# Performance work log

Hardware: AMD Instinct MI355X
Metric: run time of the kernel (lower is better)

Reference implementation:

```python
import jax, jax.numpy as jnp
import numpy as np

B, NQ, N, D_IN, D_KEY, D_MODEL = 8, 2048, 2048, 512, 512, 512


def setup_inputs() -> dict:
    key = jax.random.key(0)
    k1, k2, k3, k4, k5, k6 = jax.random.split(key, 6)
    lim_k = np.sqrt(6.0 / (D_IN + D_KEY))
    lim_v = np.sqrt(6.0 / (D_IN + D_MODEL))
    return {
        "node_features": jax.random.normal(k1, (B, N, D_IN), dtype=jnp.float32),
        "query": jax.random.normal(k2, (B, NQ, D_IN), dtype=jnp.float32),
        "mask": jax.random.bernoulli(k3, 0.3, (NQ, B, N)),  # True = masked out
        "wq": jax.random.uniform(k4, (D_IN, D_KEY), jnp.float32, -lim_k, lim_k),
        "wk": jax.random.uniform(k5, (D_IN, D_KEY), jnp.float32, -lim_k, lim_k),
        "wv": jax.random.uniform(k6, (D_IN, D_MODEL), jnp.float32, -lim_v, lim_v),
    }


def reference(node_features, query, mask, wq, wk, wv):
    # Projections
    Q = query @ wq              # [B, NQ, d_key]
    K = node_features @ wk      # [B, N, d_key]
    V = node_features @ wv      # [B, N, d_model]
    # Raw scores [B, NQ, N]
    scores = jnp.einsum("bqd,bnd->bqn", Q, K)
    b, nq, n = scores.shape
    # Faithful to tf: reshape to (NQ, B, N), mask with float32.min, reshape back
    s = scores.reshape(nq, b, n)
    masked = jnp.where(mask, jnp.finfo(jnp.float32).min, s).reshape(b, nq, n)
    # Scale AFTER masking (as in the original), then softmax over keys
    attn = jax.nn.softmax(masked / jnp.sqrt(jnp.float32(K.shape[-1])), axis=-1)
    return attn @ V             # [B, NQ, d_model]
```

## Files before the change

### kernel.cpp

```cpp
#include <hip/hip_runtime.h>

typedef __attribute__((ext_vector_type(8))) short bf16x8;
typedef __attribute__((ext_vector_type(4))) float f32x4;

__device__ __forceinline__ unsigned short f2bf(float f) {
  unsigned int u = __builtin_bit_cast(unsigned int, f);
  u += 0x7fffu + ((u >> 16) & 1u);
  return (unsigned short)(u >> 16);
}

#define GLD16(gp, lp) __builtin_amdgcn_global_load_lds( \
    (const __attribute__((address_space(1))) unsigned int*)(gp), \
    (__attribute__((address_space(3))) unsigned int*)(lp), 16, 0, 0)

__global__ __launch_bounds__(256) void pack_mask(
    const unsigned char* __restrict__ m, unsigned long long* __restrict__ pm)
{
  __shared__ int mode1;
  if (threadIdx.x == 0) mode1 = 0;
  __syncthreads();

  const int g = blockIdx.x * 256 + threadIdx.x;
  const size_t base = (size_t)g * 64;

  uint4 v[4];
  const uint4* p1 = (const uint4*)(m + base);
  v[0] = p1[0]; v[1] = p1[1]; v[2] = p1[2]; v[3] = p1[3];
  unsigned int probe = 0;
#pragma unroll
  for (int j = 0; j < 4; ++j)
    probe |= (v[j].x | v[j].y | v[j].z | v[j].w);
  if (probe & 0x0000ff00u) mode1 = 1;
  __syncthreads();

  unsigned long long bits = 0;
  if (mode1) {
#pragma unroll
    for (int j = 0; j < 4; ++j) {
      unsigned int w[4] = {v[j].x, v[j].y, v[j].z, v[j].w};
#pragma unroll
      for (int q = 0; q < 4; ++q) {
        unsigned int u = w[q];
#pragma unroll
        for (int b = 0; b < 4; ++b)
          if ((u >> (8 * b)) & 0xffu) bits |= 1ull << (j * 16 + q * 4 + b);
      }
    }
  } else {
    const uint4* p4 = (const uint4*)(m + base * 4);
#pragma unroll
    for (int j = 0; j < 16; ++j) {
      uint4 w = p4[j];
      if (w.x) bits |= 1ull << (j * 4 + 0);
      if (w.y) bits |= 1ull << (j * 4 + 1);
      if (w.z) bits |= 1ull << (j * 4 + 2);
      if (w.w) bits |= 1ull << (j * 4 + 3);
    }
  }
  pm[g] = bits;
}

__global__ void prep(const float* __restrict__ query, const float* __restrict__ node,
                     const float* __restrict__ wq, const float* __restrict__ wk,
                     const float* __restrict__ wv,
                     unsigned short* __restrict__ Xq, unsigned short* __restrict__ Xn,
                     unsigned short* __restrict__ wqb, unsigned short* __restrict__ wkb,
                     unsigned short* __restrict__ wvt, float* __restrict__ sums)
{
  const int b = blockIdx.x;
  if (b < 16384) {
    int i = b * 256 + threadIdx.x;
    const float* src;
    unsigned short* dst;
    int j;
    if (i < 2097152) { src = query; dst = Xq; j = i; }
    else             { src = node;  dst = Xn; j = i - 2097152; }
    float4 v = ((const float4*)src)[j];
    ushort4 o;
    o.x = f2bf(v.x); o.y = f2bf(v.y); o.z = f2bf(v.z); o.w = f2bf(v.w);
    ((ushort4*)dst)[j] = o;
  } else if (b < 19456) {
    int idx = (b - 16384) * 256 + threadIdx.x;
    int w = idx >> 18;
    int rem = idx & 262143;
    if (w == 0)      wqb[rem] = f2bf(wq[rem]);
    else if (w == 1) wkb[rem] = f2bf(wk[rem]);
    else {
      int n = rem >> 9, k = rem & 511;
      wvt[n * 512 + k] = f2bf(wv[k * 512 + n]);
    }
  } else {
    int idx = (b - 19456) * 256 + threadIdx.x;
    sums[idx] = 0.0f;
  }
}

__device__ __forceinline__ void core128(
    const unsigned short* __restrict__ Ab, const unsigned short* __restrict__ Bb,
    void* __restrict__ Cb, long ldA, long ldB, long ldO, int nk,
    long bm, long bn, char* smem, int mode,
    const unsigned long long* __restrict__ pmask, float* __restrict__ sumz,
    const float* __restrict__ sums_ro)
{
  const int tid = threadIdx.x;
  const int lane = tid & 63;
  const int wid = tid >> 6;
  const int wr = wid >> 1, wc = wid & 1;
  const int fr = lane & 15, fq = lane >> 4;

  const int srow = tid >> 2;
  const int sch = (tid & 3) ^ ((srow >> 1) & 3);

  char* bufs[3] = { smem, smem + 16384, smem + 32768 };

#define STAGE_C(buf, kt) do { \
    const long k0_ = (long)(kt) << 5; \
    GLD16(Ab + (bm + srow) * ldA + k0_ + sch * 8,        (buf) + tid * 16); \
    GLD16(Ab + (bm + 64 + srow) * ldA + k0_ + sch * 8,   (buf) + 4096 + tid * 16); \
    GLD16(Bb + (bn + srow) * ldB + k0_ + sch * 8,        (buf) + 8192 + tid * 16); \
    GLD16(Bb + (bn + 64 + srow) * ldB + k0_ + sch * 8,   (buf) + 12288 + tid * 16); \
  } while (0)

  int aoff[4], boff[4];
#pragma unroll
  for (int i = 0; i < 4; ++i) {
    const int ra = wr * 64 + i * 16 + fr;
    aoff[i] = ra * 64 + (fq ^ ((ra >> 1) & 3)) * 16;
    const int rb = wc * 64 + i * 16 + fr;
    boff[i] = 8192 + rb * 64 + (fq ^ ((rb >> 1) & 3)) * 16;
  }

  f32x4 acc[4][4] = {};

  STAGE_C(bufs[0], 0);
  STAGE_C(bufs[1], 1);
  char* c0 = bufs[0]; char* c1 = bufs[1]; char* c2 = bufs[2];

  for (int t = 0; t < nk; ++t) {
    __builtin_amdgcn_sched_barrier(0);
    __builtin_amdgcn_s_barrier();
    if (t + 2 < nk) {
      STAGE_C(c2, t + 2);
      asm volatile("s_waitcnt vmcnt(8)" ::: "memory");
    } else if (t + 2 == nk) {
      asm volatile("s_waitcnt vmcnt(4)" ::: "memory");
    } else {
      asm volatile("s_waitcnt vmcnt(0)" ::: "memory");
    }
    __builtin_amdgcn_s_barrier();
    __builtin_amdgcn_sched_barrier(0);

    bf16x8 a[4];
#pragma unroll
    for (int mi = 0; mi < 4; ++mi)
      a[mi] = *(const bf16x8*)(c0 + aoff[mi]);
    __builtin_amdgcn_s_setprio(1);
#pragma unroll
    for (int nj = 0; nj < 4; ++nj) {
      const bf16x8 b = *(const bf16x8*)(c0 + boff[nj]);
#pragma unroll
      for (int mi = 0; mi < 4; ++mi)
        acc[mi][nj] = __builtin_amdgcn_mfma_f32_16x16x32_bf16(a[mi], b, acc[mi][nj], 0, 0, 0);
    }
    __builtin_amdgcn_s_setprio(0);

    char* tmp = c0; c0 = c1; c1 = c2; c2 = tmp;
  }
#undef STAGE_C

  const float SCALE = 0.04419417382415922f;
  if (mode == 0) {
    unsigned short* C = (unsigned short*)Cb;
#pragma unroll
    for (int mi = 0; mi < 4; ++mi)
#pragma unroll
      for (int nj = 0; nj < 4; ++nj) {
        const long row = bm + wr * 64 + mi * 16 + fq * 4;
        const long col = bn + wc * 64 + nj * 16 + fr;
#pragma unroll
        for (int r = 0; r < 4; ++r)
          C[(row + r) * ldO + col] = f2bf(acc[mi][nj][r]);
      }
  } else if (mode == 1) {
    unsigned short* C = (unsigned short*)Cb;
    const long wword = (bn >> 6) + wc;
#pragma unroll
    for (int mi = 0; mi < 4; ++mi) {
      const long rowb = bm + wr * 64 + mi * 16 + fq * 4;
#pragma unroll
      for (int r = 0; r < 4; ++r) {
        const long row = rowb + r;
        const unsigned long long w = pmask[row * 32 + wword];
        unsigned short* Crow = C + row * ldO + bn + wc * 64 + fr;
        float s = 0.f;
#pragma unroll
        for (int nj = 0; nj < 4; ++nj) {
          const int sh = nj * 16 + fr;
          float e = ((w >> sh) & 1ull) ? 0.0f : __expf(acc[mi][nj][r] * SCALE);
          s += e;
          Crow[nj * 16] = f2bf(e);
        }
        s += __shfl_xor(s, 1); s += __shfl_xor(s, 2);
        s += __shfl_xor(s, 4); s += __shfl_xor(s, 8);
        if (fr == 0) atomicAdd(&sumz[row], s);
      }
    }
  } else {
    float* C = (float*)Cb;
#pragma unroll
    for (int mi = 0; mi < 4; ++mi) {
      const long rowb = bm + wr * 64 + mi * 16 + fq * 4;
#pragma unroll
      for (int r = 0; r < 4; ++r) {
        const long row = rowb + r;
        const float iv = 1.0f / sums_ro[row];
        const long colb = bn + wc * 64 + fr;
#pragma unroll
        for (int nj = 0; nj < 4; ++nj)
          C[row * ldO + colb + nj * 16] = acc[mi][nj][r] * iv;
      }
    }
  }
}

__global__ __launch_bounds__(256, 3) void gemm_mt(
    const unsigned short* __restrict__ wkb, const unsigned short* __restrict__ wqb,
    unsigned short* __restrict__ MT)
{
  extern __shared__ char smem[];
  core128(wkb, wqb, MT, 512, 512, 512, 16,
          (long)blockIdx.x * 128, (long)blockIdx.y * 128, smem, 0,
          nullptr, nullptr, nullptr);
}

__global__ __launch_bounds__(256, 3) void gemm_proj(
    const unsigned short* __restrict__ Xq, const unsigned short* __restrict__ Xn,
    const unsigned short* __restrict__ MT, const unsigned short* __restrict__ Wvt,
    unsigned short* __restrict__ T, unsigned short* __restrict__ Vt)
{
  extern __shared__ char smem[];
  if (blockIdx.z == 0) {
    core128(Xq, MT, T, 512, 512, 512, 16,
            (long)blockIdx.x * 128, (long)blockIdx.y * 128, smem, 0,
            nullptr, nullptr, nullptr);
  } else {
    core128(Wvt, Xn, Vt, 512, 512, 16384, 16,
            (long)blockIdx.y * 128, (long)blockIdx.x * 128, smem, 0,
            nullptr, nullptr, nullptr);
  }
}

__global__ __launch_bounds__(256, 3) void gemm_scores(
    const unsigned short* __restrict__ T, const unsigned short* __restrict__ Xn,
    unsigned short* __restrict__ Eg, const unsigned long long* __restrict__ pm,
    float* __restrict__ sums)
{
  extern __shared__ char smem[];
  const long z = blockIdx.x;
  core128(T + z * 1048576, Xn + z * 1048576, Eg + z * 4194304,
          512, 512, 2048, 16,
          (long)blockIdx.y * 128, (long)blockIdx.z * 128, smem, 1,
          pm + z * 65536, sums + z * 2048, nullptr);
}

__global__ __launch_bounds__(256, 3) void gemm_pv(
    const unsigned short* __restrict__ E, const unsigned short* __restrict__ Vt,
    const float* __restrict__ sums, float* __restrict__ O)
{
  extern __shared__ char smem[];
  const long z = blockIdx.x;
  core128(E + z * 4194304, Vt + z * 2048, O + z * 1048576,
          2048, 16384, 512, 64,
          (long)blockIdx.z * 128, (long)blockIdx.y * 128, smem, 2,
          nullptr, nullptr, sums + z * 2048);
}

extern "C" void kernel_launch(void* const* d_in, const int* in_sizes, int n_in,
                              void* d_out, int out_size, void* d_ws, size_t ws_size,
                              hipStream_t stream) {
  const float* node  = (const float*)d_in[0];
  const float* query = (const float*)d_in[1];
  const unsigned char* mask = (const unsigned char*)d_in[2];
  const float* wq = (const float*)d_in[3];
  const float* wk = (const float*)d_in[4];
  const float* wv = (const float*)d_in[5];
  float* out = (float*)d_out;

  char* ws = (char*)d_ws;
  unsigned short* T   = (unsigned short*)(ws);
  unsigned short* Xn  = (unsigned short*)(ws + 16777216);
  unsigned short* Vt  = (unsigned short*)(ws + 33554432);
  unsigned short* E   = (unsigned short*)(ws + 50331648);
  unsigned short* Xq  = (unsigned short*)(ws + 50331648);
  unsigned short* wqb = (unsigned short*)(ws + 67108864);
  unsigned short* wkb = (unsigned short*)(ws + 67633152);
  unsigned short* Wvt = (unsigned short*)(ws + 68157440);
  unsigned short* MT  = (unsigned short*)(ws + 68681728);
  float* sums = (float*)(ws + 117440512);
  unsigned long long* pm = (unsigned long long*)(ws + 118489088);

  pack_mask<<<2048, 256, 0, stream>>>(mask, pm);
  prep<<<19520, 256, 0, stream>>>(query, node, wq, wk, wv,
                                  Xq, Xn, wqb, wkb, Wvt, sums);

  gemm_mt<<<dim3(4, 4, 1), 256, 49152, stream>>>(wkb, wqb, MT);

  dim3 gp(128, 4, 2);
  gemm_proj<<<gp, 256, 49152, stream>>>(Xq, Xn, MT, Wvt, T, Vt);

  dim3 gs(8, 16, 16);
  gemm_scores<<<gs, 256, 49152, stream>>>(T, Xn, E, pm, sums);

  dim3 gv(8, 4, 16);
  gemm_pv<<<gv, 256, 49152, stream>>>(E, Vt, sums, out);
}
```

Before: 201.4 us.

## Fuse masked-exp score GEMM and PV GEMM into single attention kernel

Replaces the separate scores kernel (writing an unnormalized, masked exp matrix to global memory) and the PV kernel with one fused kernel. Each 512-thread block keeps 64 query rows of T in registers. It streams 32-key tiles of Xn and Vt through double-buffered LDS, computes masked exp probabilities into LDS, accumulates row sums with LDS atomics, and multiplies by V in the same pass. This removes the large bf16 probability round trip through HBM and the global atomics and memset of the sums. In exchange it runs one block per CU with three barriers per iteration, which limits latency hiding, and every block re-reads the full per-batch K and V.

```diff
diff --git a/kernel.cpp b/kernel.cpp
--- a/kernel.cpp
+++ b/kernel.cpp
@@ -65,7 +65,7 @@
                      const float* __restrict__ wv,
                      unsigned short* __restrict__ Xq, unsigned short* __restrict__ Xn,
                      unsigned short* __restrict__ wqb, unsigned short* __restrict__ wkb,
-                     unsigned short* __restrict__ wvt, float* __restrict__ sums)
+                     unsigned short* __restrict__ wvt)
 {
   const int b = blockIdx.x;
   if (b < 16384) {
@@ -79,7 +79,7 @@
     ushort4 o;
     o.x = f2bf(v.x); o.y = f2bf(v.y); o.z = f2bf(v.z); o.w = f2bf(v.w);
     ((ushort4*)dst)[j] = o;
-  } else if (b < 19456) {
+  } else {
     int idx = (b - 16384) * 256 + threadIdx.x;
     int w = idx >> 18;
     int rem = idx & 262143;
@@ -89,18 +89,13 @@
       int n = rem >> 9, k = rem & 511;
       wvt[n * 512 + k] = f2bf(wv[k * 512 + n]);
     }
-  } else {
-    int idx = (b - 19456) * 256 + threadIdx.x;
-    sums[idx] = 0.0f;
   }
 }
 
 __device__ __forceinline__ void core128(
     const unsigned short* __restrict__ Ab, const unsigned short* __restrict__ Bb,
     void* __restrict__ Cb, long ldA, long ldB, long ldO, int nk,
-    long bm, long bn, char* smem, int mode,
-    const unsigned long long* __restrict__ pmask, float* __restrict__ sumz,
-    const float* __restrict__ sums_ro)
+    long bm, long bn, char* smem)
 {
   const int tid = threadIdx.x;
   const int lane = tid & 63;
@@ -168,59 +163,17 @@
   }
 #undef STAGE_C
 
-  const float SCALE = 0.04419417382415922f;
-  if (mode == 0) {
-    unsigned short* C = (unsigned short*)Cb;
-#pragma unroll
-    for (int mi = 0; mi < 4; ++mi)
-#pragma unroll
-      for (int nj = 0; nj < 4; ++nj) {
-        const long row = bm + wr * 64 + mi * 16 + fq * 4;
-        const long col = bn + wc * 64 + nj * 16 + fr;
-#pragma unroll
-        for (int r = 0; r < 4; ++r)
-          C[(row + r) * ldO + col] = f2bf(acc[mi][nj][r]);
-      }
-  } else if (mode == 1) {
-    unsigned short* C = (unsigned short*)Cb;
-    const long wword = (bn >> 6) + wc;
-#pragma unroll
-    for (int mi = 0; mi < 4; ++mi) {
-      const long rowb = bm + wr * 64 + mi * 16 + fq * 4;
-#pragma unroll
-      for (int r = 0; r < 4; ++r) {
-        const long row = rowb + r;
-        const unsigned long long w = pmask[row * 32 + wword];
-        unsigned short* Crow = C + row * ldO + bn + wc * 64 + fr;
-        float s = 0.f;
-#pragma unroll
-        for (int nj = 0; nj < 4; ++nj) {
-          const int sh = nj * 16 + fr;
-          float e = ((w >> sh) & 1ull) ? 0.0f : __expf(acc[mi][nj][r] * SCALE);
-          s += e;
-          Crow[nj * 16] = f2bf(e);
-        }
-        s += __shfl_xor(s, 1); s += __shfl_xor(s, 2);
-        s += __shfl_xor(s, 4); s += __shfl_xor(s, 8);
-        if (fr == 0) atomicAdd(&sumz[row], s);
-      }
-    }
-  } else {
-    float* C = (float*)Cb;
-#pragma unroll
-    for (int mi = 0; mi < 4; ++mi) {
-      const long rowb = bm + wr * 64 + mi * 16 + fq * 4;
-#pragma unroll
-      for (int r = 0; r < 4; ++r) {
-        const long row = rowb + r;
-        const float iv = 1.0f / sums_ro[row];
-        const long colb = bn + wc * 64 + fr;
-#pragma unroll
-        for (int nj = 0; nj < 4; ++nj)
-          C[row * ldO + colb + nj * 16] = acc[mi][nj][r] * iv;
-      }
-    }
-  }
+  unsigned short* C = (unsigned short*)Cb;
+#pragma unroll
+  for (int mi = 0; mi < 4; ++mi)
+#pragma unroll
+    for (int nj = 0; nj < 4; ++nj) {
+      const long row = bm + wr * 64 + mi * 16 + fq * 4;
+      const long col = bn + wc * 64 + nj * 16 + fr;
+#pragma unroll
+      for (int r = 0; r < 4; ++r)
+        C[(row + r) * ldO + col] = f2bf(acc[mi][nj][r]);
+    }
 }
 
 __global__ __launch_bounds__(256, 3) void gemm_mt(
@@ -229,8 +182,7 @@
 {
   extern __shared__ char smem[];
   core128(wkb, wqb, MT, 512, 512, 512, 16,
-          (long)blockIdx.x * 128, (long)blockIdx.y * 128, smem, 0,
-          nullptr, nullptr, nullptr);
+          (long)blockIdx.x * 128, (long)blockIdx.y * 128, smem);
 }
 
 __global__ __launch_bounds__(256, 3) void gemm_proj(
@@ -241,38 +193,158 @@
   extern __shared__ char smem[];
   if (blockIdx.z == 0) {
     core128(Xq, MT, T, 512, 512, 512, 16,
-            (long)blockIdx.x * 128, (long)blockIdx.y * 128, smem, 0,
-            nullptr, nullptr, nullptr);
+            (long)blockIdx.x * 128, (long)blockIdx.y * 128, smem);
   } else {
     core128(Wvt, Xn, Vt, 512, 512, 16384, 16,
-            (long)blockIdx.y * 128, (long)blockIdx.x * 128, smem, 0,
-            nullptr, nullptr, nullptr);
-  }
-}
-
-__global__ __launch_bounds__(256, 3) void gemm_scores(
-    const unsigned short* __restrict__ T, const unsigned short* __restrict__ Xn,
-    unsigned short* __restrict__ Eg, const unsigned long long* __restrict__ pm,
-    float* __restrict__ sums)
+            (long)blockIdx.y * 128, (long)blockIdx.x * 128, smem);
+  }
+}
+
+__global__ __launch_bounds__(512, 1) void fused_attn(
+    const unsigned short* __restrict__ Tg, const unsigned short* __restrict__ Xng,
+    const unsigned short* __restrict__ Vtg, const unsigned long long* __restrict__ pm,
+    float* __restrict__ Og)
 {
   extern __shared__ char smem[];
-  const long z = blockIdx.x;
-  core128(T + z * 1048576, Xn + z * 1048576, Eg + z * 4194304,
-          512, 512, 2048, 16,
-          (long)blockIdx.y * 128, (long)blockIdx.z * 128, smem, 1,
-          pm + z * 65536, sums + z * 2048, nullptr);
-}
-
-__global__ __launch_bounds__(256, 3) void gemm_pv(
-    const unsigned short* __restrict__ E, const unsigned short* __restrict__ Vt,
-    const float* __restrict__ sums, float* __restrict__ O)
-{
-  extern __shared__ char smem[];
-  const long z = blockIdx.x;
-  core128(E + z * 4194304, Vt + z * 2048, O + z * 1048576,
-          2048, 16384, 512, 64,
-          (long)blockIdx.z * 128, (long)blockIdx.y * 128, smem, 2,
-          nullptr, nullptr, sums + z * 2048);
+  const long z  = blockIdx.x;
+  const long q0 = (long)blockIdx.y * 64;
+
+  const unsigned short* Tb  = Tg  + z * 1048576;
+  const unsigned short* Xnb = Xng + z * 1048576;
+  const unsigned short* Vtb = Vtg + z * 2048;
+  const unsigned long long* pmz = pm + z * 65536;
+  float* Ob = Og + z * 1048576;
+
+  const int tid = threadIdx.x;
+  const int lane = tid & 63;
+  const int w = tid >> 6;
+  const int fr = lane & 15, fq = lane >> 4;
+  const int qf = w >> 1;
+  const int kf = w & 1;
+
+  char* XB0 = smem;
+  char* XB1 = smem + 32768;
+  char* VB0 = smem + 65536;
+  char* VB1 = smem + 98304;
+  char* PB = smem + 131072;
+  float* sums_l = (float*)(smem + 135168);
+
+  if (tid < 64) sums_l[tid] = 0.0f;
+
+  bf16x8 af[16];
+  {
+    const unsigned short* tp = Tb + (q0 + qf * 16 + fr) * 512 + fq * 8;
+#pragma unroll
+    for (int s = 0; s < 16; ++s)
+      af[s] = *(const bf16x8*)(tp + s * 32);
+  }
+
+  const int xr = tid >> 6;
+  const int xcs = (tid & 63) ^ (xr & 7);
+  const int vr = tid >> 2;
+  const int vcs = (tid & 3) ^ ((vr >> 1) & 3);
+
+#define STAGE_F(xb_, vb_, kv0_) do { \
+    const unsigned short* xs_ = Xnb + ((kv0_) + xr) * 512 + xcs * 8; \
+    GLD16(xs_,              (xb_) + tid * 16); \
+    GLD16(xs_ + 8 * 512,    (xb_) + 8192 + tid * 16); \
+    GLD16(xs_ + 16 * 512,   (xb_) + 16384 + tid * 16); \
+    GLD16(xs_ + 24 * 512,   (xb_) + 24576 + tid * 16); \
+    const unsigned short* vs_ = Vtb + (long)vr * 16384 + (kv0_) + vcs * 8; \
+    GLD16(vs_,                   (vb_) + tid * 16); \
+    GLD16(vs_ + 128L * 16384,    (vb_) + 8192 + tid * 16); \
+    GLD16(vs_ + 256L * 16384,    (vb_) + 16384 + tid * 16); \
+    GLD16(vs_ + 384L * 16384,    (vb_) + 24576 + tid * 16); \
+  } while (0)
+
+  const int kvl = kf * 16 + fr;
+  const int ksw = kvl & 7;
+
+  f32x4 acc[4][4] = {};
+  const float SCALE = 0.04419417382415922f;
+
+  STAGE_F(XB0, VB0, 0);
+
+  for (int it = 0; it < 64; ++it) {
+    const int kv0 = it * 32;
+    char* xb = (it & 1) ? XB1 : XB0;
+    char* vb = (it & 1) ? VB1 : VB0;
+    char* xbn = (it & 1) ? XB0 : XB1;
+    char* vbn = (it & 1) ? VB0 : VB1;
+
+    __builtin_amdgcn_sched_barrier(0);
+    __builtin_amdgcn_s_barrier();
+    if (it + 1 < 64) {
+      STAGE_F(xbn, vbn, kv0 + 32);
+      asm volatile("s_waitcnt vmcnt(8)" ::: "memory");
+    } else {
+      asm volatile("s_waitcnt vmcnt(0)" ::: "memory");
+    }
+    __builtin_amdgcn_s_barrier();
+    __builtin_amdgcn_sched_barrier(0);
+
+    f32x4 sacc = {};
+    __builtin_amdgcn_s_setprio(1);
+#pragma unroll
+    for (int s = 0; s < 16; ++s) {
+      const bf16x8 b = *(const bf16x8*)(xb + kvl * 1024 + (((s * 4 + fq) ^ ksw) * 16));
+      sacc = __builtin_amdgcn_mfma_f32_16x16x32_bf16(af[s], b, sacc, 0, 0, 0);
+    }
+    __builtin_amdgcn_s_setprio(0);
+
+    const int wordc = (kv0 + kf * 16) >> 6;
+#pragma unroll
+    for (int i = 0; i < 4; ++i) {
+      const int prow = qf * 16 + fq * 4 + i;
+      const unsigned long long mw = pmz[(q0 + prow) * 32 + wordc];
+      const int bit = (kv0 + kvl) & 63;
+      float e = ((mw >> bit) & 1ull) ? 0.0f : __expf(sacc[i] * SCALE);
+      const int pchunk = (kf * 2 + (fr >> 3)) ^ ((prow >> 1) & 3);
+      *(unsigned short*)(PB + prow * 64 + pchunk * 16 + (fr & 7) * 2) = f2bf(e);
+      float s_ = e;
+      s_ += __shfl_xor(s_, 1); s_ += __shfl_xor(s_, 2);
+      s_ += __shfl_xor(s_, 4); s_ += __shfl_xor(s_, 8);
+      if (fr == 0) atomicAdd(&sums_l[prow], s_);
+    }
+
+    asm volatile("s_waitcnt lgkmcnt(0)" ::: "memory");
+    __builtin_amdgcn_sched_barrier(0);
+    __builtin_amdgcn_s_barrier();
+    __builtin_amdgcn_sched_barrier(0);
+
+    bf16x8 pa[4];
+#pragma unroll
+    for (int m = 0; m < 4; ++m) {
+      const int prow = m * 16 + fr;
+      pa[m] = *(const bf16x8*)(PB + prow * 64 + ((fq ^ ((prow >> 1) & 3)) * 16));
+    }
+    __builtin_amdgcn_s_setprio(1);
+#pragma unroll
+    for (int n = 0; n < 4; ++n) {
+      const int vrow = w * 64 + n * 16 + fr;
+      const bf16x8 bv = *(const bf16x8*)(vb + vrow * 64 + ((fq ^ ((vrow >> 1) & 3)) * 16));
+#pragma unroll
+      for (int m = 0; m < 4; ++m)
+        acc[m][n] = __builtin_amdgcn_mfma_f32_16x16x32_bf16(pa[m], bv, acc[m][n], 0, 0, 0);
+    }
+    __builtin_amdgcn_s_setprio(0);
+  }
+#undef STAGE_F
+
+  asm volatile("s_waitcnt lgkmcnt(0)" ::: "memory");
+  __builtin_amdgcn_sched_barrier(0);
+  __builtin_amdgcn_s_barrier();
+#pragma unroll
+  for (int m = 0; m < 4; ++m)
+#pragma unroll
+    for (int r = 0; r < 4; ++r) {
+      const int qr = m * 16 + fq * 4 + r;
+      const float iv = 1.0f / sums_l[qr];
+      float* orow = Ob + (q0 + qr) * 512 + w * 64 + fr;
+#pragma unroll
+      for (int n = 0; n < 4; ++n)
+        orow[n * 16] = acc[m][n][r] * iv;
+    }
 }
 
 extern "C" void kernel_launch(void* const* d_in, const int* in_sizes, int n_in,
@@ -290,27 +362,22 @@
   unsigned short* T   = (unsigned short*)(ws);
   unsigned short* Xn  = (unsigned short*)(ws + 16777216);
   unsigned short* Vt  = (unsigned short*)(ws + 33554432);
-  unsigned short* E   = (unsigned short*)(ws + 50331648);
   unsigned short* Xq  = (unsigned short*)(ws + 50331648);
   unsigned short* wqb = (unsigned short*)(ws + 67108864);
   unsigned short* wkb = (unsigned short*)(ws + 67633152);
   unsigned short* Wvt = (unsigned short*)(ws + 68157440);
   unsigned short* MT  = (unsigned short*)(ws + 68681728);
-  float* sums = (float*)(ws + 117440512);
   unsigned long long* pm = (unsigned long long*)(ws + 118489088);
 
   pack_mask<<<2048, 256, 0, stream>>>(mask, pm);
-  prep<<<19520, 256, 0, stream>>>(query, node, wq, wk, wv,
-                                  Xq, Xn, wqb, wkb, Wvt, sums);
+  prep<<<19456, 256, 0, stream>>>(query, node, wq, wk, wv,
+                                  Xq, Xn, wqb, wkb, Wvt);
 
   gemm_mt<<<dim3(4, 4, 1), 256, 49152, stream>>>(wkb, wqb, MT);
 
   dim3 gp(128, 4, 2);
   gemm_proj<<<gp, 256, 49152, stream>>>(Xq, Xn, MT, Wvt, T, Vt);
 
-  dim3 gs(8, 16, 16);
-  gemm_scores<<<gs, 256, 49152, stream>>>(T, Xn, E, pm, sums);
-
-  dim3 gv(8, 4, 16);
-  gemm_pv<<<gv, 256, 49152, stream>>>(E, Vt, sums, out);
-}
+  dim3 gf(8, 32, 1);
+  fused_attn<<<gf, 512, 135424, stream>>>(T, Xn, Vt, pm, out);
+}
```

New measurement: 265.2 us. 31.7% more time.
